# Optimization experiments

Measured on AMD Instinct MI355X. Metric: run time of the kernel, lower is better.

The kernel has to match this reference:

```python
import jax, jax.numpy as jnp
import numpy as np

EMBED = 1024
HEADS = 16
HEAD_DIM = EMBED // HEADS
OUT_DIM = 1024


def setup_inputs() -> dict:
    key = jax.random.key(0)
    ks = jax.random.split(key, 8)
    N, L = 2, 2048
    values = jax.random.normal(ks[0], (N, L, EMBED), dtype=jnp.float32)
    keys_t = jax.random.normal(ks[1], (N, L, EMBED), dtype=jnp.float32)
    query = jax.random.normal(ks[2], (N, L, EMBED), dtype=jnp.float32)
    s = 1.0 / np.sqrt(HEAD_DIM)
    Wv = jax.random.normal(ks[3], (HEAD_DIM, HEAD_DIM), dtype=jnp.float32) * s
    Wk = jax.random.normal(ks[4], (HEAD_DIM, HEAD_DIM), dtype=jnp.float32) * s
    Wq = jax.random.normal(ks[5], (HEAD_DIM, HEAD_DIM), dtype=jnp.float32) * s
    Wout = jax.random.normal(ks[6], (OUT_DIM, EMBED), dtype=jnp.float32) * (1.0 / np.sqrt(EMBED))
    bout = jax.random.normal(ks[7], (OUT_DIM,), dtype=jnp.float32) * 0.01
    return {"values": values, "keys": keys_t, "query": query,
            "Wv": Wv, "Wk": Wk, "Wq": Wq, "Wout": Wout, "bout": bout}


def reference(values, keys, query, Wv, Wk, Wq, Wout, bout):
    N, Lq, _ = query.shape
    Lk = keys.shape[1]
    # split into heads: (N, L, H, D)
    v = values.reshape(N, Lk, HEADS, HEAD_DIM)
    k = keys.reshape(N, Lk, HEADS, HEAD_DIM)
    q = query.reshape(N, Lq, HEADS, HEAD_DIM)
    # per-head shared linear projections (torch Linear: x @ W.T, no bias)
    v = jnp.einsum('nlhd,ed->nlhe', v, Wv)
    k = jnp.einsum('nlhd,ed->nlhe', k, Wk)
    q = jnp.einsum('nqhd,ed->nqhe', q, Wq)
    # scores (N, H, Q, K); NOTE: scale is 1/sqrt(embed_size), per original code
    scores = jnp.einsum('nqhd,nkhd->nhqk', q, k) / jnp.sqrt(jnp.float32(EMBED))
    attn = jax.nn.softmax(scores, axis=-1)
    out = jnp.einsum('nhqk,nkhd->nqhd', attn, v).reshape(N, Lq, EMBED)
    # fc_out: x @ Wout.T + bout
    return out @ Wout.T + bout
```

## Files before the change

kernel.cpp:

```cpp
#include <hip/hip_runtime.h>
#include <cstdint>

typedef __attribute__((ext_vector_type(8))) short short8;
typedef __attribute__((ext_vector_type(4))) float floatx4;
typedef __attribute__((ext_vector_type(4))) _Float16 half4;

#define DEV __device__ __forceinline__

constexpr int NB = 2, Lseq = 2048, NH = 16, HD = 64, EMB = 1024;
constexpr float QSCALE = 0.03125f * 1.4426950408889634f;

DEV uint16_t f2bf(float f) {
  uint32_t x = __builtin_bit_cast(uint32_t, f);
  x += 0x7fffu + ((x >> 16) & 1u);
  return (uint16_t)(x >> 16);
}

DEV uint32_t pack2(float lo, float hi) {
  uint32_t a = __builtin_bit_cast(uint32_t, lo) + 0x8000u;
  uint32_t b = __builtin_bit_cast(uint32_t, hi) + 0x8000u;
  return __builtin_amdgcn_perm(b, a, 0x07060302);
}

DEV uint32_t packh2(float lo, float hi) {
  return __builtin_bit_cast(uint32_t, __builtin_amdgcn_cvt_pkrtz(lo, hi));
}

DEV void gl_lds16(const void* g, void* l) {
  __builtin_amdgcn_global_load_lds((const __attribute__((address_space(1))) void*)g,
                                   (__attribute__((address_space(3))) void*)l, 16, 0, 0);
}

DEV short8 ld8bf(const float* p, float sc) {
  float4 u = *(const float4*)p;
  float4 v = *(const float4*)(p + 4);
  union { short8 s; uint32_t d[4]; } r;
  r.d[0] = pack2(u.x * sc, u.y * sc);
  r.d[1] = pack2(u.z * sc, u.w * sc);
  r.d[2] = pack2(v.x * sc, v.y * sc);
  r.d[3] = pack2(v.z * sc, v.w * sc);
  return r.s;
}

__global__ __launch_bounds__(256) void prep_kernel(
    const float* __restrict__ values, const float* __restrict__ keysrc,
    const float* __restrict__ query, const float* __restrict__ Wv,
    const float* __restrict__ Wk, const float* __restrict__ Wq,
    const float* __restrict__ Wout,
    uint16_t* __restrict__ qp, uint16_t* __restrict__ kp,
    uint16_t* __restrict__ vp, uint16_t* __restrict__ wbf) {
  const int t = threadIdx.x, w = t >> 6, lane = t & 63;
  const int quad = lane >> 4, l16 = lane & 15;
  const int wid = blockIdx.x * 4 + w;
  const int mat = wid >> 10, sub = wid & 1023;

  if (mat == 3) {
#pragma unroll
    for (int i = 0; i < 4; ++i) {
      int idx = sub * 256 + i * 64 + lane;
      float4 v = ((const float4*)Wout)[idx];
      uint2 p;
      p.x = pack2(v.x, v.y);
      p.y = pack2(v.z, v.w);
      ((uint2*)wbf)[idx] = p;
    }
    return;
  }

  floatx4 c[4][4];
#pragma unroll
  for (int i = 0; i < 4; ++i)
#pragma unroll
    for (int j = 0; j < 4; ++j) c[i][j] = floatx4{0.f, 0.f, 0.f, 0.f};

  if (mat < 2) {
    const float* src = mat ? keysrc : query;
    const float* W   = mat ? Wk : Wq;
    const float asc  = mat ? 1.f : QSCALE;
    uint16_t* dst    = mat ? kp : qp;
    const int R0 = sub * 64;
    short8 a[4][2], b[4][2];
#pragma unroll
    for (int dc = 0; dc < 2; ++dc) {
#pragma unroll
      for (int f = 0; f < 4; ++f) {
        a[f][dc] = ld8bf(W + (size_t)(f * 16 + l16) * 64 + dc * 32 + quad * 8, asc);
        b[f][dc] = ld8bf(src + (size_t)(R0 + f * 16 + l16) * 64 + dc * 32 + quad * 8, 1.f);
      }
    }
#pragma unroll
    for (int dc = 0; dc < 2; ++dc)
#pragma unroll
      for (int mf = 0; mf < 4; ++mf)
#pragma unroll
        for (int nf = 0; nf < 4; ++nf)
          c[mf][nf] = __builtin_amdgcn_mfma_f32_16x16x32_bf16(a[mf][dc], b[nf][dc], c[mf][nf], 0, 0, 0);
#pragma unroll
    for (int nf = 0; nf < 4; ++nf) {
      int r = R0 + nf * 16 + l16;
      int h = r & 15, l = (r >> 4) & 2047, n = r >> 15;
      uint16_t* drow = dst + ((size_t)(n * 16 + h) * 2048 + l) * 64;
#pragma unroll
      for (int mf = 0; mf < 4; ++mf) {
        uint2 pk;
        pk.x = pack2(c[mf][nf][0], c[mf][nf][1]);
        pk.y = pack2(c[mf][nf][2], c[mf][nf][3]);
        *(uint2*)(drow + mf * 16 + quad * 4) = pk;
      }
    }
  } else {
    const int nh = sub >> 5, L0 = (sub & 31) * 64;
    const int n = nh >> 4, h = nh & 15;
    short8 a[4][2], b[4][2];
#pragma unroll
    for (int dc = 0; dc < 2; ++dc) {
#pragma unroll
      for (int f = 0; f < 4; ++f) {
        a[f][dc] = ld8bf(values + (size_t)(n * 2048 + L0 + f * 16 + l16) * 1024 + h * 64 + dc * 32 + quad * 8, 1.f);
        b[f][dc] = ld8bf(Wv + (size_t)(f * 16 + l16) * 64 + dc * 32 + quad * 8, 1.f);
      }
    }
#pragma unroll
    for (int dc = 0; dc < 2; ++dc)
#pragma unroll
      for (int mf = 0; mf < 4; ++mf)
#pragma unroll
        for (int nf = 0; nf < 4; ++nf)
          c[mf][nf] = __builtin_amdgcn_mfma_f32_16x16x32_bf16(a[mf][dc], b[nf][dc], c[mf][nf], 0, 0, 0);
#pragma unroll
    for (int nf = 0; nf < 4; ++nf) {
      int d = nf * 16 + l16;
      uint16_t* drow = vp + ((size_t)nh * 64 + d) * 2048 + L0;
#pragma unroll
      for (int mf = 0; mf < 4; ++mf) {
        uint2 pk;
        pk.x = packh2(c[mf][nf][0], c[mf][nf][1]);
        pk.y = packh2(c[mf][nf][2], c[mf][nf][3]);
        *(uint2*)(drow + mf * 16 + quad * 4) = pk;
      }
    }
  }
}

__global__ __launch_bounds__(256, 4) void flash_kernel(const uint16_t* __restrict__ qp,
                                                       const uint16_t* __restrict__ kp,
                                                       const uint16_t* __restrict__ vp,
                                                       uint16_t* __restrict__ xg) {
  constexpr int kbn = 32;
  __shared__ uint16_t Kt[2][64 * 64];
  __shared__ uint16_t Vt[2][64 * 64];
  const int t = threadIdx.x;
  const int w = t >> 6, lane = t & 63, quad = lane >> 4, l16 = lane & 15;
  const int nh = blockIdx.x, qt = blockIdx.y;
  const int q0 = qt * 128 + w * 32;
  const uint16_t* Qb = qp + (size_t)nh * Lseq * HD;
  const uint16_t* Kb = kp + (size_t)nh * Lseq * HD;
  const uint16_t* Vb = vp + (size_t)nh * HD * Lseq;
  const int srow = lane >> 3, sc8 = (lane & 7) ^ (lane >> 3);

  short8 bq[2][2];
#pragma unroll
  for (int qb = 0; qb < 2; ++qb) {
    bq[qb][0] = *(const short8*)(Qb + (q0 + qb * 16 + l16) * 64 + quad * 8);
    bq[qb][1] = *(const short8*)(Qb + (q0 + qb * 16 + l16) * 64 + 32 + quad * 8);
  }

  floatx4 o[4][2];
  floatx4 lfr[2];
#pragma unroll
  for (int i = 0; i < 4; ++i)
#pragma unroll
    for (int qb = 0; qb < 2; ++qb) o[i][qb] = floatx4{0.f, 0.f, 0.f, 0.f};
  lfr[0] = lfr[1] = floatx4{0.f, 0.f, 0.f, 0.f};
  const _Float16 one = (_Float16)1.0f;
  const half4 vone = {one, one, one, one};

#pragma unroll
  for (int i = 0; i < 2; ++i) {
    int r0 = w * 16 + i * 8;
    gl_lds16(Kb + (r0 + srow) * 64 + sc8 * 8, &Kt[0][r0 * 64]);
    gl_lds16(Vb + (size_t)(r0 + srow) * Lseq + sc8 * 8, &Vt[0][r0 * 64]);
  }

  for (int kb = 0; kb < kbn; ++kb) {
    __syncthreads();
    const int cur = kb & 1;
    if (kb + 1 < kbn) {
      const int nxt = cur ^ 1;
      const uint16_t* kg = Kb + (kb + 1) * (64 * 64);
#pragma unroll
      for (int i = 0; i < 2; ++i) {
        int r0 = w * 16 + i * 8;
        gl_lds16(kg + (r0 + srow) * 64 + sc8 * 8, &Kt[nxt][r0 * 64]);
        gl_lds16(Vb + (size_t)(r0 + srow) * Lseq + (kb + 1) * 64 + sc8 * 8, &Vt[nxt][r0 * 64]);
      }
    }

    floatx4 s[4][2];
#pragma unroll
    for (int kb16 = 0; kb16 < 4; ++kb16)
#pragma unroll
      for (int qb = 0; qb < 2; ++qb) s[kb16][qb] = floatx4{0.f, 0.f, 0.f, 0.f};
#pragma unroll
    for (int dc = 0; dc < 2; ++dc) {
#pragma unroll
      for (int kb16 = 0; kb16 < 4; ++kb16) {
        int row = kb16 * 16 + l16;
        short8 ak = *(const short8*)(&Kt[cur][row * 64 + ((dc * 4 + quad) ^ (row & 7)) * 8]);
        s[kb16][0] = __builtin_amdgcn_mfma_f32_16x16x32_bf16(ak, bq[0][dc], s[kb16][0], 0, 0, 0);
        s[kb16][1] = __builtin_amdgcn_mfma_f32_16x16x32_bf16(ak, bq[1][dc], s[kb16][1], 0, 0, 0);
      }
    }

    half4 bp[4][2];
#pragma unroll
    for (int qb = 0; qb < 2; ++qb) {
#pragma unroll
      for (int kb16 = 0; kb16 < 4; ++kb16) {
        float p0 = __builtin_amdgcn_exp2f(s[kb16][qb][0]);
        float p1 = __builtin_amdgcn_exp2f(s[kb16][qb][1]);
        float p2 = __builtin_amdgcn_exp2f(s[kb16][qb][2]);
        float p3 = __builtin_amdgcn_exp2f(s[kb16][qb][3]);
        union { half4 h4; uint32_t d[2]; } u;
        u.d[0] = packh2(p0, p1);
        u.d[1] = packh2(p2, p3);
        bp[kb16][qb] = u.h4;
      }
    }
#pragma unroll
    for (int kb16 = 0; kb16 < 4; ++kb16) {
      lfr[0] = __builtin_amdgcn_mfma_f32_16x16x16f16(vone, bp[kb16][0], lfr[0], 0, 0, 0);
      lfr[1] = __builtin_amdgcn_mfma_f32_16x16x16f16(vone, bp[kb16][1], lfr[1], 0, 0, 0);
    }

#pragma unroll
    for (int kb16 = 0; kb16 < 4; ++kb16) {
#pragma unroll
      for (int db = 0; db < 4; ++db) {
        int row = db * 16 + l16;
        int ch = (kb16 * 2 + (quad >> 1)) ^ (row & 7);
        half4 av = *(const half4*)(&Vt[cur][row * 64 + ch * 8 + (quad & 1) * 4]);
        o[db][0] = __builtin_amdgcn_mfma_f32_16x16x16f16(av, bp[kb16][0], o[db][0], 0, 0, 0);
        o[db][1] = __builtin_amdgcn_mfma_f32_16x16x16f16(av, bp[kb16][1], o[db][1], 0, 0, 0);
      }
    }
  }

  const int nn = nh >> 4, h = nh & 15;
  const float inv0 = __builtin_amdgcn_rcpf(lfr[0][0]);
  const float inv1 = __builtin_amdgcn_rcpf(lfr[1][0]);
#pragma unroll
  for (int qb = 0; qb < 2; ++qb) {
    const float inv = qb ? inv1 : inv0;
    uint16_t* xr = xg + ((size_t)(nn * 2048 + q0 + qb * 16 + l16)) * 1024 + h * 64 + quad * 4;
#pragma unroll
    for (int db = 0; db < 4; ++db) {
      uint2 pk;
      pk.x = pack2(o[db][qb][0] * inv, o[db][qb][1] * inv);
      pk.y = pack2(o[db][qb][2] * inv, o[db][qb][3] * inv);
      *(uint2*)(xr + db * 16) = pk;
    }
  }
}

__global__ __launch_bounds__(256, 2) void out_gemm(const uint16_t* __restrict__ Xg,
                                                   const uint16_t* __restrict__ Wb,
                                                   const float* __restrict__ bias,
                                                   float* __restrict__ out) {
  __shared__ uint16_t Xt[2][64 * 64];
  __shared__ uint16_t Wt[2][128 * 64];
  const int t = threadIdx.x, w = t >> 6, lane = t & 63, quad = lane >> 4, l16 = lane & 15;
  const int m0 = blockIdx.x * 64, o0 = blockIdx.y * 128;
  const int srow = lane >> 3, sc8 = (lane & 7) ^ (lane >> 3);

  floatx4 acc[8];
#pragma unroll
  for (int j = 0; j < 8; ++j) acc[j] = floatx4{0.f, 0.f, 0.f, 0.f};

  auto stage = [&](int buf, int kt) {
#pragma unroll
    for (int i = 0; i < 2; ++i) {
      int r0 = w * 16 + i * 8;
      gl_lds16(Xg + (size_t)(m0 + r0 + srow) * 1024 + kt * 64 + sc8 * 8, &Xt[buf][r0 * 64]);
    }
#pragma unroll
    for (int i = 0; i < 4; ++i) {
      int r0 = w * 32 + i * 8;
      gl_lds16(Wb + (size_t)(o0 + r0 + srow) * 1024 + kt * 64 + sc8 * 8, &Wt[buf][r0 * 64]);
    }
  };

  stage(0, 0);

  for (int kt = 0; kt < 16; ++kt) {
    const int cur = kt & 1;
    __syncthreads();
    if (kt + 1 < 16) stage(cur ^ 1, kt + 1);
#pragma unroll
    for (int kc = 0; kc < 2; ++kc) {
      int ra = w * 16 + l16;
      short8 a = *(const short8*)(&Xt[cur][ra * 64 + ((kc * 4 + quad) ^ (ra & 7)) * 8]);
#pragma unroll
      for (int nf = 0; nf < 8; ++nf) {
        int rb = nf * 16 + l16;
        short8 b = *(const short8*)(&Wt[cur][rb * 64 + ((kc * 4 + quad) ^ (rb & 7)) * 8]);
        acc[nf] = __builtin_amdgcn_mfma_f32_16x16x32_bf16(a, b, acc[nf], 0, 0, 0);
      }
    }
  }

#pragma unroll
  for (int nf = 0; nf < 8; ++nf) {
    float bv = bias[o0 + nf * 16 + l16];
#pragma unroll
    for (int r = 0; r < 4; ++r)
      out[(size_t)(m0 + w * 16 + quad * 4 + r) * 1024 + o0 + nf * 16 + l16] = acc[nf][r] + bv;
  }
}

extern "C" void kernel_launch(void* const* d_in, const int* in_sizes, int n_in,
                              void* d_out, int out_size, void* d_ws, size_t ws_size,
                              hipStream_t stream) {
  const float* values = (const float*)d_in[0];
  const float* keys   = (const float*)d_in[1];
  const float* query  = (const float*)d_in[2];
  const float* Wv     = (const float*)d_in[3];
  const float* Wk     = (const float*)d_in[4];
  const float* Wq     = (const float*)d_in[5];
  const float* Wout   = (const float*)d_in[6];
  const float* bout   = (const float*)d_in[7];
  float* out = (float*)d_out;
  (void)ws_size;

  uint16_t* ws  = (uint16_t*)d_ws;
  uint16_t* qp  = ws;
  uint16_t* kp  = ws + (size_t)4194304;
  uint16_t* vp  = ws + (size_t)8388608;
  uint16_t* wbf = ws + (size_t)12582912;
  uint16_t* xp  = ws + (size_t)13631488;

  prep_kernel<<<dim3(1024), dim3(256), 0, stream>>>(values, keys, query, Wv, Wk, Wq, Wout,
                                                    qp, kp, vp, wbf);
  flash_kernel<<<dim3(32, 16), dim3(256), 0, stream>>>(qp, kp, vp, xp);
  out_gemm<<<dim3(64, 8), dim3(256), 0, stream>>>(xp, wbf, bout, out);
}
```

Baseline: 182.6 us.

## Triple-buffer LDS loads with explicit vmcnt waits; compute row sums with VALU

Both the flash attention kernel and the output GEMM move from double to triple buffering of the LDS tiles. They prefetch two tiles ahead and use partial s_waitcnt vmcnt plus a raw s_barrier in place of __syncthreads, so global loads stay in flight across iterations. The flash kernel also drops the ones-vector MFMA that computed softmax row sums. It accumulates the sums with scalar adds and reduces them across lanes at the end, which frees matrix-core issue slots. LDS use rises by half, which may reduce occupancy, and the hand-written vmcnt counts must match the number of loads issued per stage.

```diff
diff --git a/kernel.cpp b/kernel.cpp
--- a/kernel.cpp
+++ b/kernel.cpp
@@ -147,8 +147,8 @@
                                                        const uint16_t* __restrict__ vp,
                                                        uint16_t* __restrict__ xg) {
   constexpr int kbn = 32;
-  __shared__ uint16_t Kt[2][64 * 64];
-  __shared__ uint16_t Vt[2][64 * 64];
+  __shared__ uint16_t Kt[3][64 * 64];
+  __shared__ uint16_t Vt[3][64 * 64];
   const int t = threadIdx.x;
   const int w = t >> 6, lane = t & 63, quad = lane >> 4, l16 = lane & 15;
   const int nh = blockIdx.x, qt = blockIdx.y;
@@ -166,34 +166,32 @@
   }
 
   floatx4 o[4][2];
-  floatx4 lfr[2];
+  float lsum[2] = {0.f, 0.f};
 #pragma unroll
   for (int i = 0; i < 4; ++i)
 #pragma unroll
     for (int qb = 0; qb < 2; ++qb) o[i][qb] = floatx4{0.f, 0.f, 0.f, 0.f};
-  lfr[0] = lfr[1] = floatx4{0.f, 0.f, 0.f, 0.f};
-  const _Float16 one = (_Float16)1.0f;
-  const half4 vone = {one, one, one, one};
-
-#pragma unroll
-  for (int i = 0; i < 2; ++i) {
-    int r0 = w * 16 + i * 8;
-    gl_lds16(Kb + (r0 + srow) * 64 + sc8 * 8, &Kt[0][r0 * 64]);
-    gl_lds16(Vb + (size_t)(r0 + srow) * Lseq + sc8 * 8, &Vt[0][r0 * 64]);
-  }
-
+
+  auto issue = [&](int tile, int buf) {
+#pragma unroll
+    for (int i = 0; i < 2; ++i) {
+      int r0 = w * 16 + i * 8;
+      gl_lds16(Kb + (size_t)tile * 4096 + (r0 + srow) * 64 + sc8 * 8, &Kt[buf][r0 * 64]);
+      gl_lds16(Vb + (size_t)(r0 + srow) * Lseq + tile * 64 + sc8 * 8, &Vt[buf][r0 * 64]);
+    }
+  };
+
+  issue(0, 0);
+  issue(1, 1);
+
+  int cur = 0;
   for (int kb = 0; kb < kbn; ++kb) {
-    __syncthreads();
-    const int cur = kb & 1;
-    if (kb + 1 < kbn) {
-      const int nxt = cur ^ 1;
-      const uint16_t* kg = Kb + (kb + 1) * (64 * 64);
-#pragma unroll
-      for (int i = 0; i < 2; ++i) {
-        int r0 = w * 16 + i * 8;
-        gl_lds16(kg + (r0 + srow) * 64 + sc8 * 8, &Kt[nxt][r0 * 64]);
-        gl_lds16(Vb + (size_t)(r0 + srow) * Lseq + (kb + 1) * 64 + sc8 * 8, &Vt[nxt][r0 * 64]);
-      }
+    if (kb + 1 < kbn) asm volatile("s_waitcnt vmcnt(4)" ::: "memory");
+    else              asm volatile("s_waitcnt vmcnt(0)" ::: "memory");
+    __builtin_amdgcn_s_barrier();
+    if (kb + 2 < kbn) {
+      int tgt = cur + 2; if (tgt >= 3) tgt -= 3;
+      issue(kb + 2, tgt);
     }
 
     floatx4 s[4][2];
@@ -221,16 +219,12 @@
         float p1 = __builtin_amdgcn_exp2f(s[kb16][qb][1]);
         float p2 = __builtin_amdgcn_exp2f(s[kb16][qb][2]);
         float p3 = __builtin_amdgcn_exp2f(s[kb16][qb][3]);
+        lsum[qb] += (p0 + p1) + (p2 + p3);
         union { half4 h4; uint32_t d[2]; } u;
         u.d[0] = packh2(p0, p1);
         u.d[1] = packh2(p2, p3);
         bp[kb16][qb] = u.h4;
       }
-    }
-#pragma unroll
-    for (int kb16 = 0; kb16 < 4; ++kb16) {
-      lfr[0] = __builtin_amdgcn_mfma_f32_16x16x16f16(vone, bp[kb16][0], lfr[0], 0, 0, 0);
-      lfr[1] = __builtin_amdgcn_mfma_f32_16x16x16f16(vone, bp[kb16][1], lfr[1], 0, 0, 0);
     }
 
 #pragma unroll
@@ -244,20 +238,29 @@
         o[db][1] = __builtin_amdgcn_mfma_f32_16x16x16f16(av, bp[kb16][1], o[db][1], 0, 0, 0);
       }
     }
+
+    asm volatile("s_waitcnt lgkmcnt(0)" ::: "memory");
+    cur = (cur + 1 == 3) ? 0 : cur + 1;
+  }
+
+  float inv[2];
+#pragma unroll
+  for (int qb = 0; qb < 2; ++qb) {
+    float v = lsum[qb];
+    v += __shfl_xor(v, 16, 64);
+    v += __shfl_xor(v, 32, 64);
+    inv[qb] = __builtin_amdgcn_rcpf(v);
   }
 
   const int nn = nh >> 4, h = nh & 15;
-  const float inv0 = __builtin_amdgcn_rcpf(lfr[0][0]);
-  const float inv1 = __builtin_amdgcn_rcpf(lfr[1][0]);
 #pragma unroll
   for (int qb = 0; qb < 2; ++qb) {
-    const float inv = qb ? inv1 : inv0;
     uint16_t* xr = xg + ((size_t)(nn * 2048 + q0 + qb * 16 + l16)) * 1024 + h * 64 + quad * 4;
 #pragma unroll
     for (int db = 0; db < 4; ++db) {
       uint2 pk;
-      pk.x = pack2(o[db][qb][0] * inv, o[db][qb][1] * inv);
-      pk.y = pack2(o[db][qb][2] * inv, o[db][qb][3] * inv);
+      pk.x = pack2(o[db][qb][0] * inv[qb], o[db][qb][1] * inv[qb]);
+      pk.y = pack2(o[db][qb][2] * inv[qb], o[db][qb][3] * inv[qb]);
       *(uint2*)(xr + db * 16) = pk;
     }
   }
@@ -267,8 +270,8 @@
                                                    const uint16_t* __restrict__ Wb,
                                                    const float* __restrict__ bias,
                                                    float* __restrict__ out) {
-  __shared__ uint16_t Xt[2][64 * 64];
-  __shared__ uint16_t Wt[2][128 * 64];
+  __shared__ uint16_t Xt[3][64 * 64];
+  __shared__ uint16_t Wt[3][128 * 64];
   const int t = threadIdx.x, w = t >> 6, lane = t & 63, quad = lane >> 4, l16 = lane & 15;
   const int m0 = blockIdx.x * 64, o0 = blockIdx.y * 128;
   const int srow = lane >> 3, sc8 = (lane & 7) ^ (lane >> 3);
@@ -291,11 +294,17 @@
   };
 
   stage(0, 0);
-
+  stage(1, 1);
+
+  int cur = 0;
   for (int kt = 0; kt < 16; ++kt) {
-    const int cur = kt & 1;
-    __syncthreads();
-    if (kt + 1 < 16) stage(cur ^ 1, kt + 1);
+    if (kt + 1 < 16) asm volatile("s_waitcnt vmcnt(6)" ::: "memory");
+    else             asm volatile("s_waitcnt vmcnt(0)" ::: "memory");
+    __builtin_amdgcn_s_barrier();
+    if (kt + 2 < 16) {
+      int tgt = cur + 2; if (tgt >= 3) tgt -= 3;
+      stage(tgt, kt + 2);
+    }
 #pragma unroll
     for (int kc = 0; kc < 2; ++kc) {
       int ra = w * 16 + l16;
@@ -307,6 +316,8 @@
         acc[nf] = __builtin_amdgcn_mfma_f32_16x16x32_bf16(a, b, acc[nf], 0, 0, 0);
       }
     }
+    asm volatile("s_waitcnt lgkmcnt(0)" ::: "memory");
+    cur = (cur + 1 == 3) ? 0 : cur + 1;
   }
 
 #pragma unroll
```

Result: no change. 180.8 us (-1.0%).

## Halve flash query tile per block and triple-buffer out_gemm loads

Applied to the files above, without the earlier changes.

The flash kernel now gives each warp 16 query rows instead of 32 and launches twice as many blocks (32x32 grid). This raises parallelism and cuts register pressure, but each K/V tile is now reused across half as many queries, so K/V traffic doubles. The output GEMM moves from double to triple buffering, with explicit vmcnt waits and raw barriers so loads run two stages ahead. That adds shared memory per block and relies on hand-counted outstanding-load numbers.

```diff
diff --git a/kernel.cpp b/kernel.cpp
--- a/kernel.cpp
+++ b/kernel.cpp
@@ -152,26 +152,21 @@
   const int t = threadIdx.x;
   const int w = t >> 6, lane = t & 63, quad = lane >> 4, l16 = lane & 15;
   const int nh = blockIdx.x, qt = blockIdx.y;
-  const int q0 = qt * 128 + w * 32;
+  const int q0 = qt * 64 + w * 16;
   const uint16_t* Qb = qp + (size_t)nh * Lseq * HD;
   const uint16_t* Kb = kp + (size_t)nh * Lseq * HD;
   const uint16_t* Vb = vp + (size_t)nh * HD * Lseq;
   const int srow = lane >> 3, sc8 = (lane & 7) ^ (lane >> 3);
 
-  short8 bq[2][2];
-#pragma unroll
-  for (int qb = 0; qb < 2; ++qb) {
-    bq[qb][0] = *(const short8*)(Qb + (q0 + qb * 16 + l16) * 64 + quad * 8);
-    bq[qb][1] = *(const short8*)(Qb + (q0 + qb * 16 + l16) * 64 + 32 + quad * 8);
-  }
-
-  floatx4 o[4][2];
-  floatx4 lfr[2];
-#pragma unroll
-  for (int i = 0; i < 4; ++i)
-#pragma unroll
-    for (int qb = 0; qb < 2; ++qb) o[i][qb] = floatx4{0.f, 0.f, 0.f, 0.f};
-  lfr[0] = lfr[1] = floatx4{0.f, 0.f, 0.f, 0.f};
+  short8 bq[2];
+  bq[0] = *(const short8*)(Qb + (q0 + l16) * 64 + quad * 8);
+  bq[1] = *(const short8*)(Qb + (q0 + l16) * 64 + 32 + quad * 8);
+
+  floatx4 o[4];
+  floatx4 lfr;
+#pragma unroll
+  for (int i = 0; i < 4; ++i) o[i] = floatx4{0.f, 0.f, 0.f, 0.f};
+  lfr = floatx4{0.f, 0.f, 0.f, 0.f};
   const _Float16 one = (_Float16)1.0f;
   const half4 vone = {one, one, one, one};
 
@@ -196,42 +191,34 @@
       }
     }
 
-    floatx4 s[4][2];
-#pragma unroll
-    for (int kb16 = 0; kb16 < 4; ++kb16)
-#pragma unroll
-      for (int qb = 0; qb < 2; ++qb) s[kb16][qb] = floatx4{0.f, 0.f, 0.f, 0.f};
+    floatx4 s[4];
+#pragma unroll
+    for (int kb16 = 0; kb16 < 4; ++kb16) s[kb16] = floatx4{0.f, 0.f, 0.f, 0.f};
 #pragma unroll
     for (int dc = 0; dc < 2; ++dc) {
 #pragma unroll
       for (int kb16 = 0; kb16 < 4; ++kb16) {
         int row = kb16 * 16 + l16;
         short8 ak = *(const short8*)(&Kt[cur][row * 64 + ((dc * 4 + quad) ^ (row & 7)) * 8]);
-        s[kb16][0] = __builtin_amdgcn_mfma_f32_16x16x32_bf16(ak, bq[0][dc], s[kb16][0], 0, 0, 0);
-        s[kb16][1] = __builtin_amdgcn_mfma_f32_16x16x32_bf16(ak, bq[1][dc], s[kb16][1], 0, 0, 0);
-      }
-    }
-
-    half4 bp[4][2];
-#pragma unroll
-    for (int qb = 0; qb < 2; ++qb) {
-#pragma unroll
-      for (int kb16 = 0; kb16 < 4; ++kb16) {
-        float p0 = __builtin_amdgcn_exp2f(s[kb16][qb][0]);
-        float p1 = __builtin_amdgcn_exp2f(s[kb16][qb][1]);
-        float p2 = __builtin_amdgcn_exp2f(s[kb16][qb][2]);
-        float p3 = __builtin_amdgcn_exp2f(s[kb16][qb][3]);
-        union { half4 h4; uint32_t d[2]; } u;
-        u.d[0] = packh2(p0, p1);
-        u.d[1] = packh2(p2, p3);
-        bp[kb16][qb] = u.h4;
-      }
-    }
+        s[kb16] = __builtin_amdgcn_mfma_f32_16x16x32_bf16(ak, bq[dc], s[kb16], 0, 0, 0);
+      }
+    }
+
+    half4 bp[4];
 #pragma unroll
     for (int kb16 = 0; kb16 < 4; ++kb16) {
-      lfr[0] = __builtin_amdgcn_mfma_f32_16x16x16f16(vone, bp[kb16][0], lfr[0], 0, 0, 0);
-      lfr[1] = __builtin_amdgcn_mfma_f32_16x16x16f16(vone, bp[kb16][1], lfr[1], 0, 0, 0);
-    }
+      float p0 = __builtin_amdgcn_exp2f(s[kb16][0]);
+      float p1 = __builtin_amdgcn_exp2f(s[kb16][1]);
+      float p2 = __builtin_amdgcn_exp2f(s[kb16][2]);
+      float p3 = __builtin_amdgcn_exp2f(s[kb16][3]);
+      union { half4 h4; uint32_t d[2]; } u;
+      u.d[0] = packh2(p0, p1);
+      u.d[1] = packh2(p2, p3);
+      bp[kb16] = u.h4;
+    }
+#pragma unroll
+    for (int kb16 = 0; kb16 < 4; ++kb16)
+      lfr = __builtin_amdgcn_mfma_f32_16x16x16f16(vone, bp[kb16], lfr, 0, 0, 0);
 
 #pragma unroll
     for (int kb16 = 0; kb16 < 4; ++kb16) {
@@ -240,26 +227,20 @@
         int row = db * 16 + l16;
         int ch = (kb16 * 2 + (quad >> 1)) ^ (row & 7);
         half4 av = *(const half4*)(&Vt[cur][row * 64 + ch * 8 + (quad & 1) * 4]);
-        o[db][0] = __builtin_amdgcn_mfma_f32_16x16x16f16(av, bp[kb16][0], o[db][0], 0, 0, 0);
-        o[db][1] = __builtin_amdgcn_mfma_f32_16x16x16f16(av, bp[kb16][1], o[db][1], 0, 0, 0);
+        o[db] = __builtin_amdgcn_mfma_f32_16x16x16f16(av, bp[kb16], o[db], 0, 0, 0);
       }
     }
   }
 
   const int nn = nh >> 4, h = nh & 15;
-  const float inv0 = __builtin_amdgcn_rcpf(lfr[0][0]);
-  const float inv1 = __builtin_amdgcn_rcpf(lfr[1][0]);
-#pragma unroll
-  for (int qb = 0; qb < 2; ++qb) {
-    const float inv = qb ? inv1 : inv0;
-    uint16_t* xr = xg + ((size_t)(nn * 2048 + q0 + qb * 16 + l16)) * 1024 + h * 64 + quad * 4;
-#pragma unroll
-    for (int db = 0; db < 4; ++db) {
-      uint2 pk;
-      pk.x = pack2(o[db][qb][0] * inv, o[db][qb][1] * inv);
-      pk.y = pack2(o[db][qb][2] * inv, o[db][qb][3] * inv);
-      *(uint2*)(xr + db * 16) = pk;
-    }
+  const float inv = __builtin_amdgcn_rcpf(lfr[0]);
+  uint16_t* xr = xg + ((size_t)(nn * 2048 + q0 + l16)) * 1024 + h * 64 + quad * 4;
+#pragma unroll
+  for (int db = 0; db < 4; ++db) {
+    uint2 pk;
+    pk.x = pack2(o[db][0] * inv, o[db][1] * inv);
+    pk.y = pack2(o[db][2] * inv, o[db][3] * inv);
+    *(uint2*)(xr + db * 16) = pk;
   }
 }
 
@@ -267,8 +248,8 @@
                                                    const uint16_t* __restrict__ Wb,
                                                    const float* __restrict__ bias,
                                                    float* __restrict__ out) {
-  __shared__ uint16_t Xt[2][64 * 64];
-  __shared__ uint16_t Wt[2][128 * 64];
+  __shared__ uint16_t Xt[3][64 * 64];
+  __shared__ uint16_t Wt[3][128 * 64];
   const int t = threadIdx.x, w = t >> 6, lane = t & 63, quad = lane >> 4, l16 = lane & 15;
   const int m0 = blockIdx.x * 64, o0 = blockIdx.y * 128;
   const int srow = lane >> 3, sc8 = (lane & 7) ^ (lane >> 3);
@@ -291,11 +272,17 @@
   };
 
   stage(0, 0);
-
+  stage(1, 1);
+
+  int cur = 0;
   for (int kt = 0; kt < 16; ++kt) {
-    const int cur = kt & 1;
-    __syncthreads();
-    if (kt + 1 < 16) stage(cur ^ 1, kt + 1);
+    if (kt + 1 < 16) asm volatile("s_waitcnt vmcnt(6)" ::: "memory");
+    else             asm volatile("s_waitcnt vmcnt(0)" ::: "memory");
+    __builtin_amdgcn_s_barrier();
+    if (kt + 2 < 16) {
+      int tgt = cur + 2; if (tgt >= 3) tgt -= 3;
+      stage(tgt, kt + 2);
+    }
 #pragma unroll
     for (int kc = 0; kc < 2; ++kc) {
       int ra = w * 16 + l16;
@@ -307,6 +294,8 @@
         acc[nf] = __builtin_amdgcn_mfma_f32_16x16x32_bf16(a, b, acc[nf], 0, 0, 0);
       }
     }
+    asm volatile("s_waitcnt lgkmcnt(0)" ::: "memory");
+    cur = (cur + 1 == 3) ? 0 : cur + 1;
   }
 
 #pragma unroll
@@ -341,6 +330,6 @@
 
   prep_kernel<<<dim3(1024), dim3(256), 0, stream>>>(values, keys, query, Wv, Wk, Wq, Wout,
                                                     qp, kp, vp, wbf);
-  flash_kernel<<<dim3(32, 16), dim3(256), 0, stream>>>(qp, kp, vp, xp);
+  flash_kernel<<<dim3(32, 32), dim3(256), 0, stream>>>(qp, kp, vp, xp);
   out_gemm<<<dim3(64, 8), dim3(256), 0, stream>>>(xp, wbf, bout, out);
 }
```

Result: faster. 176.5 us (-3.4%).
